# Kernel optimization log

Measured on AMD Instinct MI355X. Metric: run time of the kernel, lower is better.

Reference implementation:

```python
import jax, jax.numpy as jnp
import numpy as np

DEPTH = 8
N_NODES = 2 ** DEPTH - 1   # 255
N_LEAVES = 2 ** DEPTH      # 256
BATCH = 512


def _build_matrices(depth):
    """Replicates TreeMapping.__init__ mask construction exactly."""
    n = 2 ** depth - 1
    matches = []

    def recurse_(curr_depth, rm, lm, i):
        if curr_depth == depth:
            matches.append((rm, lm))
            return
        rm1 = rm.copy(); lm1 = lm.copy(); rm1[i] = 1; lm1[i] = 0
        rm2 = rm.copy(); lm2 = lm.copy(); rm2[i] = 0; lm2[i] = 1
        recurse_(curr_depth + 1, rm1, lm1, 2 * i + 1)      # right subtree first (matches torch order)
        recurse_(curr_depth + 1, rm2, lm2, 2 * (i + 1))    # left subtree

    recurse_(0, [0] * n, [0] * n, 0)
    leaf_right = np.array([m[0] for m in matches], dtype=np.float32)  # [n_leaves, n]
    leaf_left = np.array([m[1] for m in matches], dtype=np.float32)
    leaf_no = np.ones_like(leaf_left)
    leaf_no[leaf_left == 1] = 0
    leaf_no[leaf_right == 1] = 0

    right_m = np.zeros((n, n), dtype=np.float32)
    left_m = np.zeros((n, n), dtype=np.float32)

    def node_recurse(idx, parent, right_parent):
        if idx >= n:
            return
        if parent is not None:
            pr = right_m[parent].copy(); pl = left_m[parent].copy()
            if right_parent:
                pr[parent] = 1; pl[parent] = 0
            else:
                pr[parent] = 0; pl[parent] = 1
            right_m[idx] = pr; left_m[idx] = pl
        node_recurse(2 * idx + 1, idx, True)
        node_recurse(2 * (idx + 1), idx, False)

    node_recurse(0, None, False)
    no_m = np.ones((n, n), dtype=np.float32)
    no_m[left_m == 1] = 0
    no_m[right_m == 1] = 0

    combined_right = np.vstack([leaf_right, right_m])  # [n_leaves + n, n]
    combined_left = np.vstack([leaf_left, left_m])
    combined_no = np.vstack([leaf_no, no_m])
    return combined_right, combined_left, combined_no


def setup_inputs() -> dict:
    key = jax.random.key(0)
    x = jax.random.uniform(key, (BATCH, N_NODES), dtype=jnp.float32)  # routing probs in [0,1]
    cr, cl, cn = _build_matrices(DEPTH)
    return {
        "x": x,
        "right_bin": jnp.asarray(cr),
        "left_bin": jnp.asarray(cl),
        "no_bin": jnp.asarray(cn),
    }


def reference(x, right_bin, left_bin, no_bin):
    # comb: [B, n_leaves + n_nodes, n_nodes]
    comb = (x[:, None, :] * right_bin[None]
            + (1.0 - x)[:, None, :] * left_bin[None]
            + no_bin[None])
    path_prob = jnp.prod(comb, axis=-1)  # [B, n_leaves + n_nodes]
    leaf_probs = path_prob[:, :N_LEAVES]
    node_probs = path_prob[:, N_LEAVES:]
    return leaf_probs, node_probs
```

## Files before the change

kernel.cpp:

```cpp
#include <hip/hip_runtime.h>


#define TM_BATCH    512
#define TM_N_NODES  255
#define TM_N_LEAVES 256
#define TM_DEPTH    8

__global__ __launch_bounds__(256)
void TreeMapping_67671504715946_kernel(const float* __restrict__ x,
                                       float* __restrict__ out) {
    __shared__ float xs[TM_N_LEAVES];
    const int b = blockIdx.x;
    const int t = threadIdx.x;

    if (t < TM_N_NODES) xs[t] = x[b * TM_N_NODES + t];
    __syncthreads();

    float* __restrict__ leaf_out = out;
    float* __restrict__ node_out = out + TM_BATCH * TM_N_LEAVES;

    float f[TM_DEPTH];
#pragma unroll
    for (int d = 0; d < TM_DEPTH; ++d) {
        const int i = (1 << d) - 1 + (t >> (TM_DEPTH - d));
        const float xv = xs[i];
        const int bit = (t >> (TM_DEPTH - 1 - d)) & 1;
        f[d] = bit ? (1.0f - xv) : xv;
    }

    float p = 1.0f;
#pragma unroll
    for (int d = 0; d < TM_DEPTH; ++d) {
        if ((t & ((TM_N_LEAVES >> d) - 1)) == 0) {
            node_out[b * TM_N_NODES + (1 << d) - 1 + (t >> (TM_DEPTH - d))] = p;
        }
        p *= f[d];
    }
    leaf_out[b * TM_N_LEAVES + t] = p;
}

extern "C" void kernel_launch(void* const* d_in, const int* in_sizes, int n_in,
                              void* d_out, int out_size, void* d_ws, size_t ws_size,
                              hipStream_t stream) {
    const float* x = (const float*)d_in[0];
    float* out = (float*)d_out;

    TreeMapping_67671504715946_kernel<<<TM_BATCH, 256, 0, stream>>>(x, out);
}
```

Baseline: 59.69 us.

## Process four batch rows per block with one wavefront per row and float4 leaf stores

Each block now handles four batch rows, with one 64-lane wavefront per row instead of 256 threads per row. Each lane walks the first six tree levels, then expands its subtree's last two levels in registers and writes four leaves with a single float4 store. This cuts the block count and per-thread redundant shared loads and multiplies, and widens the leaf stores. In exchange the grid shrinks to 128 blocks, which may underfill the GPU, and the node stores in the last levels become strided.

```diff
diff --git a/kernel.cpp b/kernel.cpp
--- a/kernel.cpp
+++ b/kernel.cpp
@@ -4,39 +4,55 @@
 #define TM_BATCH    512
 #define TM_N_NODES  255
 #define TM_N_LEAVES 256
-#define TM_DEPTH    8
+#define TM_ROWS_PB  4
 
 __global__ __launch_bounds__(256)
 void TreeMapping_67671504715946_kernel(const float* __restrict__ x,
                                        float* __restrict__ out) {
-    __shared__ float xs[TM_N_LEAVES];
-    const int b = blockIdx.x;
-    const int t = threadIdx.x;
+    __shared__ float xs[TM_ROWS_PB][TM_N_LEAVES];
+    const int t    = threadIdx.x;
+    const int rr   = t >> 6;
+    const int lane = t & 63;
+    const int row  = blockIdx.x * TM_ROWS_PB + rr;
 
-    if (t < TM_N_NODES) xs[t] = x[b * TM_N_NODES + t];
+    const float* __restrict__ xrow = x + row * TM_N_NODES;
+#pragma unroll
+    for (int k = 0; k < 4; ++k) {
+        const int idx = lane + 64 * k;
+        if (idx < TM_N_NODES) xs[rr][idx] = xrow[idx];
+    }
     __syncthreads();
 
-    float* __restrict__ leaf_out = out;
-    float* __restrict__ node_out = out + TM_BATCH * TM_N_LEAVES;
-
-    float f[TM_DEPTH];
-#pragma unroll
-    for (int d = 0; d < TM_DEPTH; ++d) {
-        const int i = (1 << d) - 1 + (t >> (TM_DEPTH - d));
-        const float xv = xs[i];
-        const int bit = (t >> (TM_DEPTH - 1 - d)) & 1;
-        f[d] = bit ? (1.0f - xv) : xv;
-    }
+    float* __restrict__ leaf_out = out + row * TM_N_LEAVES;
+    float* __restrict__ node_out = out + TM_BATCH * TM_N_LEAVES + row * TM_N_NODES;
 
     float p = 1.0f;
 #pragma unroll
-    for (int d = 0; d < TM_DEPTH; ++d) {
-        if ((t & ((TM_N_LEAVES >> d) - 1)) == 0) {
-            node_out[b * TM_N_NODES + (1 << d) - 1 + (t >> (TM_DEPTH - d))] = p;
-        }
-        p *= f[d];
+    for (int d = 0; d < 6; ++d) {
+        const int i = (1 << d) - 1 + (lane >> (6 - d));
+        const float xv = xs[rr][i];
+        if ((lane & ((64 >> d) - 1)) == 0) node_out[i] = p;
+        const int bit = (lane >> (5 - d)) & 1;
+        p *= bit ? (1.0f - xv) : xv;
     }
-    leaf_out[b * TM_N_LEAVES + t] = p;
+    const float C = p;
+
+    const float x6  = xs[rr][63 + lane];
+    const float x7a = xs[rr][127 + 2 * lane];
+    const float x7b = xs[rr][128 + 2 * lane];
+
+    node_out[63 + lane] = C;
+    const float C6a = C * x6;
+    const float C6b = C * (1.0f - x6);
+    node_out[127 + 2 * lane] = C6a;
+    node_out[128 + 2 * lane] = C6b;
+
+    float4 lv;
+    lv.x = C6a * x7a;
+    lv.y = C6a * (1.0f - x7a);
+    lv.z = C6b * x7b;
+    lv.w = C6b * (1.0f - x7b);
+    *reinterpret_cast<float4*>(leaf_out + 4 * lane) = lv;
 }
 
 extern "C" void kernel_launch(void* const* d_in, const int* in_sizes, int n_in,
@@ -45,5 +61,5 @@
     const float* x = (const float*)d_in[0];
     float* out = (float*)d_out;
 
-    TreeMapping_67671504715946_kernel<<<TM_BATCH, 256, 0, stream>>>(x, out);
+    TreeMapping_67671504715946_kernel<<<TM_BATCH / TM_ROWS_PB, 256, 0, stream>>>(x, out);
 }
```

Measured after the change: 59.93 us. Within noise of the previous version (+0.4%).
